# Kernel tuning notes

Measured on AMD Instinct MI355X. Metric: run time of the kernel, lower is better.

Reference implementation:

```python
import jax, jax.numpy as jnp
import numpy as np

D_MODEL = 1024
NUM_HEADS = 16
D_K = D_MODEL // NUM_HEADS


def setup_inputs() -> dict:
    key = jax.random.key(0)
    ks = jax.random.split(key, 11)
    B, S = 2, 2048
    scale = 1.0 / np.sqrt(D_MODEL)
    return {
        "Q": jax.random.normal(ks[0], (B, S, D_MODEL), jnp.float32),
        "K": jax.random.normal(ks[1], (B, S, D_MODEL), jnp.float32),
        "V": jax.random.normal(ks[2], (B, S, D_MODEL), jnp.float32),
        "Wq": jax.random.normal(ks[3], (D_MODEL, D_MODEL), jnp.float32) * scale,
        "bq": jnp.zeros((D_MODEL,), jnp.float32),
        "Wk": jax.random.normal(ks[4], (D_MODEL, D_MODEL), jnp.float32) * scale,
        "bk": jnp.zeros((D_MODEL,), jnp.float32),
        "Wv": jax.random.normal(ks[5], (D_MODEL, D_MODEL), jnp.float32) * scale,
        "bv": jnp.zeros((D_MODEL,), jnp.float32),
        "Wo": jax.random.normal(ks[6], (D_MODEL, D_MODEL), jnp.float32) * scale,
        "bo": jnp.zeros((D_MODEL,), jnp.float32),
    }


def reference(Q, K, V, Wq, bq, Wk, bk, Wv, bv, Wo, bo):
    B, S, _ = Q.shape
    # linear projections (torch Linear: x @ W.T + b)
    q = Q @ Wq.T + bq
    k = K @ Wk.T + bk
    v = V @ Wv.T + bv
    # split heads: [B, S, H, d_k] -> [B, H, S, d_k]
    q = q.reshape(B, S, NUM_HEADS, D_K).transpose(0, 2, 1, 3)
    k = k.reshape(B, S, NUM_HEADS, D_K).transpose(0, 2, 1, 3)
    v = v.reshape(B, S, NUM_HEADS, D_K).transpose(0, 2, 1, 3)
    # scaled dot-product attention, full [B, H, S, S] scores as in original
    scores = jnp.einsum("bhqd,bhkd->bhqk", q, k) / jnp.sqrt(jnp.float32(D_K))
    probs = jax.nn.softmax(scores, axis=-1)
    attn = jnp.einsum("bhqk,bhkd->bhqd", probs, v)
    # merge heads and output projection
    attn = attn.transpose(0, 2, 1, 3).reshape(B, S, D_MODEL)
    return attn @ Wo.T + bo
```

## Files before the change

kernel.cpp:

```cpp
#include <hip/hip_runtime.h>
#include <cstdint>
#include <cstddef>

#define D_MODEL 1024
#define NHEADS 16
#define DK 64
#define BATCH 2
#define SEQ 2048
#define MROWS 4096

using f32x4 = __attribute__((ext_vector_type(4))) float;
using f32x16 = __attribute__((ext_vector_type(16))) float;
using u16x8 = __attribute__((ext_vector_type(8))) unsigned short;
using u32x4 = __attribute__((ext_vector_type(4))) unsigned int;
using bf16x8 = __attribute__((ext_vector_type(8))) __bf16;

static __device__ __forceinline__ f32x4 mfma16(u16x8 a, u16x8 b, f32x4 c) {
    return __builtin_amdgcn_mfma_f32_16x16x32_bf16(
        __builtin_bit_cast(bf16x8, a), __builtin_bit_cast(bf16x8, b), c, 0, 0, 0);
}
static __device__ __forceinline__ f32x16 mfma32(u16x8 a, u16x8 b, f32x16 c) {
    return __builtin_amdgcn_mfma_f32_32x32x16_bf16(
        __builtin_bit_cast(bf16x8, a), __builtin_bit_cast(bf16x8, b), c, 0, 0, 0);
}

static __device__ __forceinline__ unsigned short f2b(float f) {
    unsigned int u = __float_as_uint(f);
    u += 0x7fffu + ((u >> 16) & 1u);
    return (unsigned short)(u >> 16);
}
static __device__ __forceinline__ unsigned int cvt_pk(float lo, float hi) {
    unsigned int r;
    asm("v_cvt_pk_bf16_f32 %0, %1, %2" : "=v"(r) : "v"(lo), "v"(hi));
    return r;
}
static __device__ __forceinline__ void plswap(unsigned int& a, unsigned int& b) {
    asm("v_permlane32_swap_b32 %0, %1" : "+v"(a), "+v"(b));
}
static __device__ __forceinline__ float fexp2(float x) {
#if __has_builtin(__builtin_amdgcn_exp2f)
    return __builtin_amdgcn_exp2f(x);
#else
    float r;
    asm("v_exp_f32 %0, %1" : "=v"(r) : "v"(x));
    return r;
#endif
}
static __device__ __forceinline__ void gll16(const void* g, void* l) {
    __builtin_amdgcn_global_load_lds(
        (const __attribute__((address_space(1))) void*)g,
        (__attribute__((address_space(3))) void*)l, 16, 0, 0);
}
#define SBAR() __builtin_amdgcn_s_barrier()
#define SCHED0() __builtin_amdgcn_sched_barrier(0)

__global__ __launch_bounds__(256) void cvtw_kernel(const float* __restrict__ w0,
                                                   const float* __restrict__ w1,
                                                   const float* __restrict__ w2,
                                                   const float* __restrict__ w3,
                                                   unsigned short* __restrict__ out,
                                                   int n4, float scale0) {
    const float* srcs[4] = {w0, w1, w2, w3};
    const float* src = srcs[blockIdx.y];
    unsigned short* dst = out + (size_t)blockIdx.y * (size_t)n4 * 4;
    float scale = (blockIdx.y == 0) ? scale0 : 1.0f;
    int i = blockIdx.x * 256 + threadIdx.x;
    if (i < n4) {
        float4 v = reinterpret_cast<const float4*>(src)[i];
        ushort4 o;
        o.x = f2b(v.x * scale);
        o.y = f2b(v.y * scale);
        o.z = f2b(v.z * scale);
        o.w = f2b(v.w * scale);
        reinterpret_cast<ushort4*>(dst)[i] = o;
    }
}

__global__ __launch_bounds__(256) void cvta_kernel(const float* __restrict__ a0,
                                                   const float* __restrict__ a1,
                                                   const float* __restrict__ a2,
                                                   unsigned short* __restrict__ out,
                                                   int n4) {
    const float* srcs[3] = {a0, a1, a2};
    const float* src = srcs[blockIdx.y];
    unsigned short* dst = out + (size_t)blockIdx.y * (size_t)n4 * 4;
    int i = blockIdx.x * 256 + threadIdx.x;
    if (i < n4) {
        float4 v = reinterpret_cast<const float4*>(src)[i];
        ushort4 o;
        o.x = f2b(v.x);
        o.y = f2b(v.y);
        o.z = f2b(v.z);
        o.w = f2b(v.w);
        reinterpret_cast<ushort4*>(dst)[i] = o;
    }
}


__global__ __launch_bounds__(256, 4) void gemm_qkv_kernel(
    const unsigned short* __restrict__ Abf,
    const unsigned short* __restrict__ W,
    unsigned short* __restrict__ qo, unsigned short* __restrict__ ko,
    unsigned short* __restrict__ vto,
    const float* __restrict__ b0, const float* __restrict__ b1, const float* __restrict__ b2,
    float qsc) {
    __shared__ __align__(16) char Ab[2][8192];
    __shared__ __align__(16) char Wb[2][8192];

    const int tid = threadIdx.x;
    const int lane = tid & 63;
    const int wid = tid >> 6;
    const int wr = wid >> 1, wc = wid & 1;
    const int g = (lane >> 4) & 3, l16 = lane & 15;

    const int logical = ((int)blockIdx.x & 7) * 96 + ((int)blockIdx.x >> 3);
    const int m = logical >> 8;
    const int rem = logical & 255;
    const int y = rem >> 3, xc = rem & 7;
    const int row0 = y * 128;
    const int arow0 = m * MROWS + row0;
    const int wrow0 = m * 1024 + xc * 128;

    const int sline = tid >> 3;
    const int sgl = (tid & 7) ^ (sline & 7);
    const int srow = sline * 2 + (sgl >> 2);
    const int skcol = (sgl & 3) * 8;

    auto stage = [&](int k0, int buf) {
        const char* a0 = (const char*)Abf + (size_t)(arow0 + srow) * 2048 + (size_t)(k0 + skcol) * 2;
        gll16(a0, Ab[buf] + wid * 1024);
        gll16(a0 + (size_t)64 * 2048, Ab[buf] + 4096 + wid * 1024);
        const char* w0 = (const char*)W + (size_t)(wrow0 + srow) * 2048 + (size_t)(k0 + skcol) * 2;
        gll16(w0, Wb[buf] + wid * 1024);
        gll16(w0 + (size_t)64 * 2048, Wb[buf] + 4096 + wid * 1024);
    };

    const int rswz = ((((l16 & 1) << 2) + g) ^ ((l16 >> 1) & 7)) << 4;
    const int abase = (wr * 32 + (l16 >> 1)) * 128 + rswz;
    const int bbase = (wc * 32 + (l16 >> 1)) * 128 + rswz;

    f32x4 acc[4][4] = {};
    stage(0, 0);

    for (int t = 0; t < 32; ++t) {
        if (t < 31) stage((t + 1) * 32, (t & 1) ^ 1);
        if (t < 31) asm volatile("s_waitcnt vmcnt(4)" ::: "memory");
        else asm volatile("s_waitcnt vmcnt(0)" ::: "memory");
        SCHED0();
        SBAR();
        SCHED0();
        u16x8 af[4], bf[4];
#pragma unroll
        for (int mi = 0; mi < 4; ++mi)
            af[mi] = *reinterpret_cast<const u16x8*>(Ab[t & 1] + abase + mi * 1024);
#pragma unroll
        for (int ni = 0; ni < 4; ++ni)
            bf[ni] = *reinterpret_cast<const u16x8*>(Wb[t & 1] + bbase + ni * 1024);
        __builtin_amdgcn_s_setprio(1);
#pragma unroll
        for (int mi = 0; mi < 4; ++mi)
#pragma unroll
            for (int ni = 0; ni < 4; ++ni)
                acc[mi][ni] = mfma16(af[mi], bf[ni], acc[mi][ni]);
        __builtin_amdgcn_s_setprio(0);
        SBAR();
        SCHED0();
    }

    const float* bias = (m == 0) ? b0 : ((m == 1) ? b1 : b2);
    const float bsc = (m == 0) ? qsc : 1.0f;
#pragma unroll
    for (int mi = 0; mi < 4; ++mi) {
#pragma unroll
        for (int ni = 0; ni < 4; ++ni) {
            int r = row0 + wr * 64 + mi * 16 + g * 4;
            int cl = xc * 128 + wc * 64 + ni * 16 + l16;
            float bv = bsc * bias[cl];
            if (m < 2) {
                unsigned short* outp = m ? ko : qo;
#pragma unroll
                for (int j = 0; j < 4; ++j)
                    outp[(size_t)(r + j) * 1024 + cl] = f2b(acc[mi][ni][j] + bv);
            } else {
                ushort4 o;
                o.x = f2b(acc[mi][ni][0] + bv);
                o.y = f2b(acc[mi][ni][1] + bv);
                o.z = f2b(acc[mi][ni][2] + bv);
                o.w = f2b(acc[mi][ni][3] + bv);
                *reinterpret_cast<ushort4*>(vto + (size_t)cl * MROWS + r) = o;
            }
        }
    }
}

__global__ __launch_bounds__(256, 4) void gemm_out_kernel(
    const unsigned short* __restrict__ Abf,
    const unsigned short* __restrict__ W,
    float* __restrict__ fo,
    const float* __restrict__ bias) {
    __shared__ __align__(16) char Ab[2][8192];
    __shared__ __align__(16) char Wb[2][8192];

    const int tid = threadIdx.x;
    const int lane = tid & 63;
    const int wid = tid >> 6;
    const int wr = wid >> 1, wc = wid & 1;
    const int g = (lane >> 4) & 3, l16 = lane & 15;

    const int logical = ((int)blockIdx.x & 7) * 32 + ((int)blockIdx.x >> 3);
    const int y = logical >> 3, xc = logical & 7;
    const int row0 = y * 128;
    const int wrow0 = xc * 128;

    const int sline = tid >> 3;
    const int sgl = (tid & 7) ^ (sline & 7);
    const int srow = sline * 2 + (sgl >> 2);
    const int skcol = (sgl & 3) * 8;

    auto stage = [&](int k0, int buf) {
        const char* a0 = (const char*)Abf + (size_t)(row0 + srow) * 2048 + (size_t)(k0 + skcol) * 2;
        gll16(a0, Ab[buf] + wid * 1024);
        gll16(a0 + (size_t)64 * 2048, Ab[buf] + 4096 + wid * 1024);
        const char* w0 = (const char*)W + (size_t)(wrow0 + srow) * 2048 + (size_t)(k0 + skcol) * 2;
        gll16(w0, Wb[buf] + wid * 1024);
        gll16(w0 + (size_t)64 * 2048, Wb[buf] + 4096 + wid * 1024);
    };

    const int rswz = ((((l16 & 1) << 2) + g) ^ ((l16 >> 1) & 7)) << 4;
    const int abase = (wr * 32 + (l16 >> 1)) * 128 + rswz;
    const int bbase = (wc * 32 + (l16 >> 1)) * 128 + rswz;

    f32x4 acc[4][4] = {};
    stage(0, 0);

    for (int t = 0; t < 32; ++t) {
        if (t < 31) stage((t + 1) * 32, (t & 1) ^ 1);
        if (t < 31) asm volatile("s_waitcnt vmcnt(4)" ::: "memory");
        else asm volatile("s_waitcnt vmcnt(0)" ::: "memory");
        SCHED0();
        SBAR();
        SCHED0();
        u16x8 af[4], bf[4];
#pragma unroll
        for (int mi = 0; mi < 4; ++mi)
            af[mi] = *reinterpret_cast<const u16x8*>(Ab[t & 1] + abase + mi * 1024);
#pragma unroll
        for (int ni = 0; ni < 4; ++ni)
            bf[ni] = *reinterpret_cast<const u16x8*>(Wb[t & 1] + bbase + ni * 1024);
        __builtin_amdgcn_s_setprio(1);
#pragma unroll
        for (int mi = 0; mi < 4; ++mi)
#pragma unroll
            for (int ni = 0; ni < 4; ++ni)
                acc[mi][ni] = mfma16(af[mi], bf[ni], acc[mi][ni]);
        __builtin_amdgcn_s_setprio(0);
        SBAR();
        SCHED0();
    }

#pragma unroll
    for (int mi = 0; mi < 4; ++mi) {
#pragma unroll
        for (int ni = 0; ni < 4; ++ni) {
            int r = row0 + wr * 64 + mi * 16 + g * 4;
            int cl = xc * 128 + wc * 64 + ni * 16 + l16;
            float bv = bias[cl];
#pragma unroll
            for (int j = 0; j < 4; ++j)
                fo[(size_t)(r + j) * 1024 + cl] = acc[mi][ni][j] + bv;
        }
    }
}

__global__ __launch_bounds__(512, 2) void attn_kernel(
    const unsigned short* __restrict__ qp,
    const unsigned short* __restrict__ kp,
    const unsigned short* __restrict__ vT,
    unsigned short* __restrict__ ao) {
    __shared__ __align__(16) char lds[65536];

    const int tid = threadIdx.x;
    const int lane = tid & 63;
    const int wid = tid >> 6;
    const int wq = wid & 3, wk = wid >> 2;
    const int l31 = lane & 31, hi = lane >> 5;

    const int logical = ((int)blockIdx.x & 7) * 64 + ((int)blockIdx.x >> 3);
    const int qt = logical & 15;
    const int bh = logical >> 4;
    const int b = bh >> 4, h = bh & 15;
    const int ch = h * DK;
    const int q0 = b * SEQ + qt * 128;

    const int srow = wid * 8 + (lane >> 3);
    const int g16 = (lane & 7) ^ (lane >> 3);
    const char* kbase = (const char*)kp + ((size_t)(b * SEQ + srow)) * 2048 + ch * 2 + g16 * 16;
    const char* vbase = (const char*)vT + ((size_t)(ch + srow)) * (MROWS * 2) + (size_t)b * SEQ * 2 + g16 * 16;

    const char* qr = (const char*)qp + (size_t)(q0 + wq * 32 + l31) * 2048 + ch * 2;
    u16x8 qf[4];
#pragma unroll
    for (int t = 0; t < 4; ++t)
        qf[t] = *reinterpret_cast<const u16x8*>(qr + t * 32 + hi * 16);

    auto stageKV = [&](int kt2, char* base) {
        gll16(kbase + (size_t)kt2 * (64 * 2048), base + wid * 1024);
        gll16(kbase + (size_t)(kt2 * 64 + 1024) * 2048, base + 8192 + wid * 1024);
        gll16(vbase + kt2 * 128, base + 16384 + wid * 1024);
        gll16(vbase + kt2 * 128 + 2048, base + 24576 + wid * 1024);
    };

    const int swz = (lane & 7) << 4;
    f32x16 acco[2] = {};
    float l0 = 0.f, l1 = 0.f, l2 = 0.f, l3 = 0.f;

    stageKV(0, lds);
    for (int kt = 0; kt < 16; ++kt) {
        if (kt < 15) stageKV(kt + 1, lds + (((kt + 1) & 1) << 15));
        if (kt < 15) asm volatile("s_waitcnt vmcnt(4)" ::: "memory");
        else asm volatile("s_waitcnt vmcnt(0)" ::: "memory");
        SCHED0();
        SBAR();
        SCHED0();
        const char* cb = lds + ((kt & 1) << 15);
        const char* Kb = cb + wk * 8192;
        const char* Vb = cb + 16384 + wk * 8192;

        unsigned int pf[4][4];
#pragma unroll
        for (int ts = 0; ts < 2; ++ts) {
            f32x16 s = {};
            __builtin_amdgcn_s_setprio(1);
#pragma unroll
            for (int t = 0; t < 4; ++t) {
                u16x8 kf = *reinterpret_cast<const u16x8*>(Kb + (ts * 32 + l31) * 128 + ((32 * t + 16 * hi) ^ swz));
                s = mfma32(kf, qf[t], s);
            }
            __builtin_amdgcn_s_setprio(0);
            float p[16];
#pragma unroll
            for (int r = 0; r < 16; r += 4) {
                p[r] = fexp2(s[r]);
                p[r + 1] = fexp2(s[r + 1]);
                p[r + 2] = fexp2(s[r + 2]);
                p[r + 3] = fexp2(s[r + 3]);
                l0 += p[r];
                l1 += p[r + 1];
                l2 += p[r + 2];
                l3 += p[r + 3];
            }
#pragma unroll
            for (int i = 0; i < 2; ++i) {
                unsigned int a = cvt_pk(p[2 * i], p[2 * i + 1]);
                unsigned int bb = cvt_pk(p[4 + 2 * i], p[5 + 2 * i]);
                plswap(a, bb);
                pf[2 * ts][i] = a;
                pf[2 * ts][i + 2] = bb;
                unsigned int a2 = cvt_pk(p[8 + 2 * i], p[9 + 2 * i]);
                unsigned int b2 = cvt_pk(p[12 + 2 * i], p[13 + 2 * i]);
                plswap(a2, b2);
                pf[2 * ts + 1][i] = a2;
                pf[2 * ts + 1][i + 2] = b2;
            }
        }
        __builtin_amdgcn_s_setprio(1);
#pragma unroll
        for (int t = 0; t < 4; ++t) {
            u32x4 wv = {pf[t][0], pf[t][1], pf[t][2], pf[t][3]};
            u16x8 pfr = __builtin_bit_cast(u16x8, wv);
#pragma unroll
            for (int dt = 0; dt < 2; ++dt) {
                u16x8 vf = *reinterpret_cast<const u16x8*>(Vb + (dt * 32 + l31) * 128 + ((32 * t + 16 * hi) ^ swz));
                acco[dt] = mfma32(vf, pfr, acco[dt]);
            }
        }
        __builtin_amdgcn_s_setprio(0);
        SBAR();
        SCHED0();
    }

    float L = (l0 + l1) + (l2 + l3);

    float Lh = L + __shfl_xor(L, 32);
    float* cmb = reinterpret_cast<float*>(lds);
    float* slot = cmb + (size_t)tid * 18;
    f32x16 outg = acco[1 ^ wk];
#pragma unroll
    for (int mm = 0; mm < 8; ++mm)
        *reinterpret_cast<float2*>(slot + 2 * mm) = float2{outg[2 * mm], outg[2 * mm + 1]};
    slot[16] = Lh;
    __syncthreads();
    const float* ps = cmb + (size_t)(tid ^ 256) * 18;
    f32x16 kept = acco[wk];
#pragma unroll
    for (int mm = 0; mm < 8; ++mm) {
        float2 t2 = *reinterpret_cast<const float2*>(ps + 2 * mm);
        kept[2 * mm] += t2.x;
        kept[2 * mm + 1] += t2.y;
    }
    float rl = 1.0f / (Lh + ps[16]);
    __syncthreads();

    char* ot = lds + wid * 2304;
    const int r7 = l31 & 7;
#pragma unroll
    for (int mm = 0; mm < 4; ++mm) {
        uint2 pko;
        pko.x = cvt_pk(kept[4 * mm] * rl, kept[4 * mm + 1] * rl);
        pko.y = cvt_pk(kept[4 * mm + 2] * rl, kept[4 * mm + 3] * rl);
        *reinterpret_cast<uint2*>(ot + l31 * 72 + (((2 * mm + hi) ^ r7) << 3)) = pko;
    }
    const int rr = lane >> 1, half = lane & 1;
    const int rb7 = rr & 7;
    uint2 t0 = *reinterpret_cast<const uint2*>(ot + rr * 72 + (((half * 4 + 0) ^ rb7) << 3));
    uint2 t1 = *reinterpret_cast<const uint2*>(ot + rr * 72 + (((half * 4 + 1) ^ rb7) << 3));
    uint2 t2 = *reinterpret_cast<const uint2*>(ot + rr * 72 + (((half * 4 + 2) ^ rb7) << 3));
    uint2 t3 = *reinterpret_cast<const uint2*>(ot + rr * 72 + (((half * 4 + 3) ^ rb7) << 3));
    unsigned short* dst = ao + (size_t)(q0 + wq * 32 + rr) * 1024 + ch + wk * 32 + half * 16;
    uint4 o0 = {t0.x, t0.y, t1.x, t1.y};
    uint4 o1 = {t2.x, t2.y, t3.x, t3.y};
    *reinterpret_cast<uint4*>(dst) = o0;
    *reinterpret_cast<uint4*>(dst + 8) = o1;
}

extern "C" void kernel_launch(void* const* d_in, const int* in_sizes, int n_in,
                              void* d_out, int out_size, void* d_ws, size_t ws_size,
                              hipStream_t stream) {
    const float* Q = (const float*)d_in[0];
    const float* K = (const float*)d_in[1];
    const float* V = (const float*)d_in[2];
    const float* Wq = (const float*)d_in[3];
    const float* bq = (const float*)d_in[4];
    const float* Wk = (const float*)d_in[5];
    const float* bk = (const float*)d_in[6];
    const float* Wv = (const float*)d_in[7];
    const float* bv = (const float*)d_in[8];
    const float* Wo = (const float*)d_in[9];
    const float* bo = (const float*)d_in[10];

    unsigned short* ws = (unsigned short*)d_ws;
    const size_t SZ = (size_t)MROWS * D_MODEL;
    const size_t WSZ = (size_t)D_MODEL * D_MODEL;
    unsigned short* bufW = ws;
    unsigned short* abf = bufW + 4 * WSZ;
    unsigned short* qp = abf + 3 * SZ;
    unsigned short* kp = qp + SZ;
    unsigned short* vT = kp + SZ;
    unsigned short* ao = vT + SZ;

    const float qscale = 0.125f * 1.44269504088896f;

    dim3 blk(256);
    dim3 gcw((unsigned)(WSZ / 4 / 256), 4);
    cvtw_kernel<<<gcw, blk, 0, stream>>>(Wq, Wk, Wv, Wo, bufW, (int)(WSZ / 4), qscale);
    dim3 gca((unsigned)(SZ / 4 / 256), 3);
    cvta_kernel<<<gca, blk, 0, stream>>>(Q, K, V, abf, (int)(SZ / 4));

    gemm_qkv_kernel<<<dim3(768), blk, 0, stream>>>(abf, bufW, qp, kp, vT, bq, bk, bv, qscale);

    attn_kernel<<<dim3(512), dim3(512), 0, stream>>>(qp, kp, vT, ao);

    gemm_out_kernel<<<dim3(256), blk, 0, stream>>>(ao, bufW + 3 * WSZ, (float*)d_out, bo);
}
```

Measured before the change: 132.1 us.

## Fuse activation fp32-to-bf16 conversion into QKV GEMM; split output GEMM tiles

Removes the separate activation conversion kernel. The QKV GEMM now loads fp32 Q/K/V rows into registers, converts them to bf16 and writes them into a single-buffered swizzled LDS tile, with the next tile's loads overlapping the current MFMA work. This drops a full write and re-read of the bf16 activation buffer and one launch, at the cost of more VGPR pressure (occupancy hint lowered to 3) and an extra barrier per iteration. Separately, the output GEMM uses 128x64 tiles with 512 blocks to better fill the CUs.

```diff
diff --git a/kernel.cpp b/kernel.cpp
--- a/kernel.cpp
+++ b/kernel.cpp
@@ -76,35 +76,15 @@
     }
 }
 
-__global__ __launch_bounds__(256) void cvta_kernel(const float* __restrict__ a0,
-                                                   const float* __restrict__ a1,
-                                                   const float* __restrict__ a2,
-                                                   unsigned short* __restrict__ out,
-                                                   int n4) {
-    const float* srcs[3] = {a0, a1, a2};
-    const float* src = srcs[blockIdx.y];
-    unsigned short* dst = out + (size_t)blockIdx.y * (size_t)n4 * 4;
-    int i = blockIdx.x * 256 + threadIdx.x;
-    if (i < n4) {
-        float4 v = reinterpret_cast<const float4*>(src)[i];
-        ushort4 o;
-        o.x = f2b(v.x);
-        o.y = f2b(v.y);
-        o.z = f2b(v.z);
-        o.w = f2b(v.w);
-        reinterpret_cast<ushort4*>(dst)[i] = o;
-    }
-}
-
-
-__global__ __launch_bounds__(256, 4) void gemm_qkv_kernel(
-    const unsigned short* __restrict__ Abf,
+
+__global__ __launch_bounds__(256, 3) void gemm_qkv_kernel(
+    const float* __restrict__ A0, const float* __restrict__ A1, const float* __restrict__ A2,
     const unsigned short* __restrict__ W,
     unsigned short* __restrict__ qo, unsigned short* __restrict__ ko,
     unsigned short* __restrict__ vto,
     const float* __restrict__ b0, const float* __restrict__ b1, const float* __restrict__ b2,
     float qsc) {
-    __shared__ __align__(16) char Ab[2][8192];
+    __shared__ __align__(16) char Asb[8192];
     __shared__ __align__(16) char Wb[2][8192];
 
     const int tid = threadIdx.x;
@@ -118,18 +98,41 @@
     const int rem = logical & 255;
     const int y = rem >> 3, xc = rem & 7;
     const int row0 = y * 128;
-    const int arow0 = m * MROWS + row0;
     const int wrow0 = m * 1024 + xc * 128;
+
+    const float* Af = (m == 0) ? A0 : ((m == 1) ? A1 : A2);
+
+    const int arow = tid >> 1;
+    const int ahalf = tid & 1;
+    const float* asrc = Af + (size_t)(row0 + arow) * 1024 + ahalf * 16;
+    const int aline = tid >> 2;
+    const int apar = (tid >> 1) & 1;
+    const int al7 = aline & 7;
+    const int aglo = ((apar * 4 + ahalf * 2) ^ al7) * 16;
+    const int aghi = ((apar * 4 + ahalf * 2 + 1) ^ al7) * 16;
 
     const int sline = tid >> 3;
     const int sgl = (tid & 7) ^ (sline & 7);
     const int srow = sline * 2 + (sgl >> 2);
     const int skcol = (sgl & 3) * 8;
 
-    auto stage = [&](int k0, int buf) {
-        const char* a0 = (const char*)Abf + (size_t)(arow0 + srow) * 2048 + (size_t)(k0 + skcol) * 2;
-        gll16(a0, Ab[buf] + wid * 1024);
-        gll16(a0 + (size_t)64 * 2048, Ab[buf] + 4096 + wid * 1024);
+    float4 a0r, a1r, a2r, a3r;
+    auto loadA = [&](int k0) {
+        const float4* s = reinterpret_cast<const float4*>(asrc + k0);
+        a0r = s[0];
+        a1r = s[1];
+        a2r = s[2];
+        a3r = s[3];
+    };
+    auto writeA = [&]() {
+        u32x4 glo = {cvt_pk(a0r.x, a0r.y), cvt_pk(a0r.z, a0r.w),
+                     cvt_pk(a1r.x, a1r.y), cvt_pk(a1r.z, a1r.w)};
+        u32x4 ghi = {cvt_pk(a2r.x, a2r.y), cvt_pk(a2r.z, a2r.w),
+                     cvt_pk(a3r.x, a3r.y), cvt_pk(a3r.z, a3r.w)};
+        *reinterpret_cast<u32x4*>(Asb + aline * 128 + aglo) = glo;
+        *reinterpret_cast<u32x4*>(Asb + aline * 128 + aghi) = ghi;
+    };
+    auto stageW = [&](int k0, int buf) {
         const char* w0 = (const char*)W + (size_t)(wrow0 + srow) * 2048 + (size_t)(k0 + skcol) * 2;
         gll16(w0, Wb[buf] + wid * 1024);
         gll16(w0 + (size_t)64 * 2048, Wb[buf] + 4096 + wid * 1024);
@@ -140,19 +143,30 @@
     const int bbase = (wc * 32 + (l16 >> 1)) * 128 + rswz;
 
     f32x4 acc[4][4] = {};
-    stage(0, 0);
+
+    loadA(0);
+    stageW(0, 0);
+    asm volatile("s_waitcnt vmcnt(2)" ::: "memory");
+    SCHED0();
+    writeA();
+    asm volatile("s_waitcnt lgkmcnt(0)" ::: "memory");
+    SCHED0();
 
     for (int t = 0; t < 32; ++t) {
-        if (t < 31) stage((t + 1) * 32, (t & 1) ^ 1);
-        if (t < 31) asm volatile("s_waitcnt vmcnt(4)" ::: "memory");
-        else asm volatile("s_waitcnt vmcnt(0)" ::: "memory");
+        if (t < 31) {
+            loadA((t + 1) * 32);
+            stageW((t + 1) * 32, (t & 1) ^ 1);
+            asm volatile("s_waitcnt vmcnt(6)" ::: "memory");
+        } else {
+            asm volatile("s_waitcnt vmcnt(0)" ::: "memory");
+        }
         SCHED0();
         SBAR();
         SCHED0();
         u16x8 af[4], bf[4];
 #pragma unroll
         for (int mi = 0; mi < 4; ++mi)
-            af[mi] = *reinterpret_cast<const u16x8*>(Ab[t & 1] + abase + mi * 1024);
+            af[mi] = *reinterpret_cast<const u16x8*>(Asb + abase + mi * 1024);
 #pragma unroll
         for (int ni = 0; ni < 4; ++ni)
             bf[ni] = *reinterpret_cast<const u16x8*>(Wb[t & 1] + bbase + ni * 1024);
@@ -163,8 +177,15 @@
             for (int ni = 0; ni < 4; ++ni)
                 acc[mi][ni] = mfma16(af[mi], bf[ni], acc[mi][ni]);
         __builtin_amdgcn_s_setprio(0);
-        SBAR();
-        SCHED0();
+        if (t < 31) {
+            SBAR();
+            SCHED0();
+            asm volatile("s_waitcnt vmcnt(2)" ::: "memory");
+            SCHED0();
+            writeA();
+            asm volatile("s_waitcnt lgkmcnt(0)" ::: "memory");
+            SCHED0();
+        }
     }
 
     const float* bias = (m == 0) ? b0 : ((m == 1) ? b1 : b2);
@@ -199,7 +220,7 @@
     float* __restrict__ fo,
     const float* __restrict__ bias) {
     __shared__ __align__(16) char Ab[2][8192];
-    __shared__ __align__(16) char Wb[2][8192];
+    __shared__ __align__(16) char Wb[2][4096];
 
     const int tid = threadIdx.x;
     const int lane = tid & 63;
@@ -207,10 +228,10 @@
     const int wr = wid >> 1, wc = wid & 1;
     const int g = (lane >> 4) & 3, l16 = lane & 15;
 
-    const int logical = ((int)blockIdx.x & 7) * 32 + ((int)blockIdx.x >> 3);
-    const int y = logical >> 3, xc = logical & 7;
+    const int logical = ((int)blockIdx.x & 7) * 64 + ((int)blockIdx.x >> 3);
+    const int y = logical >> 4, xc = logical & 15;
     const int row0 = y * 128;
-    const int wrow0 = xc * 128;
+    const int wrow0 = xc * 64;
 
     const int sline = tid >> 3;
     const int sgl = (tid & 7) ^ (sline & 7);
@@ -223,35 +244,34 @@
         gll16(a0 + (size_t)64 * 2048, Ab[buf] + 4096 + wid * 1024);
         const char* w0 = (const char*)W + (size_t)(wrow0 + srow) * 2048 + (size_t)(k0 + skcol) * 2;
         gll16(w0, Wb[buf] + wid * 1024);
-        gll16(w0 + (size_t)64 * 2048, Wb[buf] + 4096 + wid * 1024);
     };
 
     const int rswz = ((((l16 & 1) << 2) + g) ^ ((l16 >> 1) & 7)) << 4;
     const int abase = (wr * 32 + (l16 >> 1)) * 128 + rswz;
-    const int bbase = (wc * 32 + (l16 >> 1)) * 128 + rswz;
-
-    f32x4 acc[4][4] = {};
+    const int bbase = (wc * 16 + (l16 >> 1)) * 128 + rswz;
+
+    f32x4 acc[4][2] = {};
     stage(0, 0);
 
     for (int t = 0; t < 32; ++t) {
         if (t < 31) stage((t + 1) * 32, (t & 1) ^ 1);
-        if (t < 31) asm volatile("s_waitcnt vmcnt(4)" ::: "memory");
+        if (t < 31) asm volatile("s_waitcnt vmcnt(3)" ::: "memory");
         else asm volatile("s_waitcnt vmcnt(0)" ::: "memory");
         SCHED0();
         SBAR();
         SCHED0();
-        u16x8 af[4], bf[4];
+        u16x8 af[4], bf[2];
 #pragma unroll
         for (int mi = 0; mi < 4; ++mi)
             af[mi] = *reinterpret_cast<const u16x8*>(Ab[t & 1] + abase + mi * 1024);
 #pragma unroll
-        for (int ni = 0; ni < 4; ++ni)
+        for (int ni = 0; ni < 2; ++ni)
             bf[ni] = *reinterpret_cast<const u16x8*>(Wb[t & 1] + bbase + ni * 1024);
         __builtin_amdgcn_s_setprio(1);
 #pragma unroll
         for (int mi = 0; mi < 4; ++mi)
 #pragma unroll
-            for (int ni = 0; ni < 4; ++ni)
+            for (int ni = 0; ni < 2; ++ni)
                 acc[mi][ni] = mfma16(af[mi], bf[ni], acc[mi][ni]);
         __builtin_amdgcn_s_setprio(0);
         SBAR();
@@ -261,9 +281,9 @@
 #pragma unroll
     for (int mi = 0; mi < 4; ++mi) {
 #pragma unroll
-        for (int ni = 0; ni < 4; ++ni) {
+        for (int ni = 0; ni < 2; ++ni) {
             int r = row0 + wr * 64 + mi * 16 + g * 4;
-            int cl = xc * 128 + wc * 64 + ni * 16 + l16;
+            int cl = xc * 64 + wc * 32 + ni * 16 + l16;
             float bv = bias[cl];
 #pragma unroll
             for (int j = 0; j < 4; ++j)
@@ -442,8 +462,7 @@
     const size_t SZ = (size_t)MROWS * D_MODEL;
     const size_t WSZ = (size_t)D_MODEL * D_MODEL;
     unsigned short* bufW = ws;
-    unsigned short* abf = bufW + 4 * WSZ;
-    unsigned short* qp = abf + 3 * SZ;
+    unsigned short* qp = bufW + 4 * WSZ;
     unsigned short* kp = qp + SZ;
     unsigned short* vT = kp + SZ;
     unsigned short* ao = vT + SZ;
@@ -453,12 +472,10 @@
     dim3 blk(256);
     dim3 gcw((unsigned)(WSZ / 4 / 256), 4);
     cvtw_kernel<<<gcw, blk, 0, stream>>>(Wq, Wk, Wv, Wo, bufW, (int)(WSZ / 4), qscale);
-    dim3 gca((unsigned)(SZ / 4 / 256), 3);
-    cvta_kernel<<<gca, blk, 0, stream>>>(Q, K, V, abf, (int)(SZ / 4));
-
-    gemm_qkv_kernel<<<dim3(768), blk, 0, stream>>>(abf, bufW, qp, kp, vT, bq, bk, bv, qscale);
+
+    gemm_qkv_kernel<<<dim3(768), blk, 0, stream>>>(Q, K, V, bufW, qp, kp, vT, bq, bk, bv, qscale);
 
     attn_kernel<<<dim3(512), dim3(512), 0, stream>>>(qp, kp, vT, ao);
 
-    gemm_out_kernel<<<dim3(256), blk, 0, stream>>>(ao, bufW + 3 * WSZ, (float*)d_out, bo);
-}
+    gemm_out_kernel<<<dim3(512), blk, 0, stream>>>(ao, bufW + 3 * WSZ, (float*)d_out, bo);
+}
```

Result: faster. 129.2 us (-2.1%).
